# Kernel tuning notes

Measured on AMD Instinct MI355X. Metric: run time of the kernel, lower is better.

## Reference

```python
import jax, jax.numpy as jnp
import numpy as np

THETA = 128.0


def _make_Q(d, units):
    # Q[n,m] = (2n+1)/sqrt(d) if n > m and (n+m) odd, else 0 (fixed, non-trainable)
    n = np.arange(d)[:, None]
    m = np.arange(units)[None, :]
    Q = np.where((n > m) & (((n + m) % 2) == 1), (2 * n + 1) / np.sqrt(d), 0.0)
    return jnp.asarray(Q, dtype=jnp.float32)


def setup_inputs() -> dict:
    key = jax.random.key(0)
    k1, k2, k3, k4 = jax.random.split(key, 4)
    B_, T, Din, d, units = 16, 4096, 128, 256, 256
    x = jax.random.normal(k1, (B_, T, Din), dtype=jnp.float32)
    A = jax.random.normal(k2, (d, d), dtype=jnp.float32) / np.sqrt(d)
    Bm = jax.random.normal(k3, (Din, d), dtype=jnp.float32) / np.sqrt(Din)
    W_mix = jax.random.normal(k4, (units, units), dtype=jnp.float32) / np.sqrt(units)
    b_mix = jnp.zeros((units,), dtype=jnp.float32)
    return {"x": x, "A": A, "B": Bm, "W_mix": W_mix, "b_mix": b_mix}


def reference(x, A, B, W_mix, b_mix):
    d = A.shape[0]
    units = W_mix.shape[0]
    Q = _make_Q(d, units)
    QW = Q @ W_mix  # fuse fixed projection with dense kernel: (d, units)
    alpha = 1.0 - 1.0 / THETA
    beta = 1.0 / THETA
    # precompute input projection for all steps: (T, batch, d)
    xB = jnp.einsum('bti,id->tbd', x, B)

    def step(state, xBt):
        new_state = alpha * state + beta * (state @ A + xBt)
        y = jnp.tanh(new_state @ QW + b_mix)
        return new_state, y

    s0 = jnp.zeros((x.shape[0], d), dtype=x.dtype)
    _, ys = jax.lax.scan(step, s0, xB)  # ys: (T, batch, units)
    return jnp.transpose(ys, (1, 0, 2))
```

## Files before the change

### kernel.cpp

```cpp
#include <hip/hip_runtime.h>
#include <math.h>

constexpr int T_   = 4096;
constexpr int NB   = 16;
constexpr int D_   = 256;
constexpr int DIN  = 128;
constexpr int U_   = 256;
constexpr int L1   = 8;
constexpr int C1   = T_ / L1;
constexpr float ALPHA_ = 1.0f - 1.0f / 128.0f;
constexpr float BETA_  = 1.0f / 128.0f;
constexpr int SD   = NB * D_;
constexpr int MS   = D_ * D_;
constexpr int TLP  = D_ + 4;
constexpr int XLP  = DIN + 4;

using short8  = __attribute__((ext_vector_type(8))) short;
using float4v = __attribute__((ext_vector_type(4))) float;

__device__ __forceinline__ unsigned short bf16_rne(float x) {
  const unsigned b = __float_as_uint(x);
  const unsigned r = ((b >> 16) & 1u) + 0x7FFFu;
  return (unsigned short)((b + r) >> 16);
}
__device__ __forceinline__ float bf16_f(unsigned short h) {
  return __uint_as_float(((unsigned)h) << 16);
}

__device__ __forceinline__ void split2(float e0, float e1, unsigned& hd, unsigned& ld) {
  const unsigned b0 = __float_as_uint(e0), b1 = __float_as_uint(e1);
  const unsigned h0 = b0 & 0xFFFF0000u, h1 = b1 & 0xFFFF0000u;
  const float l0 = e0 - __uint_as_float(h0);
  const float l1 = e1 - __uint_as_float(h1);
  hd = (h0 >> 16) | h1;
  ld = (__float_as_uint(l0) >> 16) | (__float_as_uint(l1) & 0xFFFF0000u);
}

__device__ __forceinline__ void unpack8(uint4 a, uint4 b, short8& hi, short8& lo) {
  union { short8 s; unsigned u[4]; } H, L;
  const unsigned d[8] = {a.x, a.y, a.z, a.w, b.x, b.y, b.z, b.w};
#pragma unroll
  for (int i = 0; i < 4; ++i) {
    H.u[i] = (d[2 * i] >> 16) | (d[2 * i + 1] & 0xFFFF0000u);
    L.u[i] = (d[2 * i] & 0xFFFFu) | (d[2 * i + 1] << 16);
  }
  hi = H.s; lo = L.s;
}

__device__ __forceinline__ void mm_row(const float* __restrict__ Am,
                                       const float* __restrict__ Bm,
                                       float* __restrict__ Dm,
                                       int i, int tid, float* srow) {
  srow[tid] = Am[i * D_ + tid];
  __syncthreads();
  float a0 = 0.f, a1 = 0.f, a2 = 0.f, a3 = 0.f;
#pragma unroll 8
  for (int k = 0; k < D_; k += 4) {
    a0 = fmaf(srow[k + 0], Bm[(k + 0) * D_ + tid], a0);
    a1 = fmaf(srow[k + 1], Bm[(k + 1) * D_ + tid], a1);
    a2 = fmaf(srow[k + 2], Bm[(k + 2) * D_ + tid], a2);
    a3 = fmaf(srow[k + 3], Bm[(k + 3) * D_ + tid], a3);
  }
  Dm[i * D_ + tid] = (a0 + a1) + (a2 + a3);
  __syncthreads();
}

__global__ __launch_bounds__(256) void k_prep(const float* __restrict__ A,
                                              const float* __restrict__ W,
                                              float* __restrict__ Meff,
                                              float* __restrict__ QW,
                                              const float* __restrict__ Bm,
                                              unsigned short* __restrict__ Mf,
                                              unsigned short* __restrict__ Bmf) {
  const int bid = blockIdx.x, tid = threadIdx.x;
  if (bid < D_) {
    float v = BETA_ * A[bid * D_ + tid];
    if (bid == tid) v += ALPHA_;
    Meff[bid * D_ + tid] = v;
    return;
  }
  if (bid == D_) {
    __shared__ float wch[32 * D_];
    float se = 0.f, so = 0.f;
    for (int ch = 0; ch < D_ / 32; ++ch) {
      __syncthreads();
      for (int idx = tid; idx < 32 * D_; idx += 256)
        wch[idx] = W[ch * 32 * D_ + idx];
      __syncthreads();
#pragma unroll
      for (int r = 0; r < 32; ++r) {
        const int n = ch * 32 + r;
        const float sum = (n & 1) ? se : so;
        QW[n * U_ + tid] = sum * ((float)(2 * n + 1) / 16.0f);
        const float wv = wch[r * D_ + tid];
        if (n & 1) so += wv; else se += wv;
      }
    }
    return;
  }
  const int pb = bid - D_ - 1;
  const int lane = tid & 63, nb0 = tid >> 6;
  const int quad = lane >> 4, m16 = lane & 15;
  if (pb < 8) {
    const int ks = pb;
    for (int nb = nb0; nb < 16; nb += 4) {
      const size_t fo = ((size_t)(nb * 8 + ks) * 64 + lane) * 8;
#pragma unroll
      for (int jj = 0; jj < 8; ++jj) {
        const int k = ks * 32 + quad * 8 + jj;
        const int n = nb * 16 + m16;
        const float v = BETA_ * A[k * D_ + n];
        const unsigned short h = bf16_rne(v);
        Mf[fo + jj] = h;
        Mf[MS + fo + jj] = bf16_rne(v - bf16_f(h));
      }
    }
  } else {
    const int ks = pb - 8;
    unsigned short* dh = Bmf;
    unsigned short* dl = Bmf + (MS / 2);
    for (int nb = nb0; nb < 16; nb += 4) {
      const size_t fo = ((size_t)(nb * 4 + ks) * 64 + lane) * 8;
#pragma unroll
      for (int jj = 0; jj < 8; ++jj) {
        const int k = ks * 32 + quad * 8 + jj;
        const int n = nb * 16 + m16;
        const float v = BETA_ * Bm[k * D_ + n];
        const unsigned short h = bf16_rne(v);
        dh[fo + jj] = h;
        dl[fo + jj] = bf16_rne(v - bf16_f(h));
      }
    }
  }
}

__global__ __launch_bounds__(256) void k_pw(const float* __restrict__ Am,
                                            const float* __restrict__ Bbase,
                                            float* __restrict__ Dbase) {
  __shared__ float srow[D_];
  const int q = blockIdx.x >> 8, row = blockIdx.x & 255;
  mm_row(Am, Bbase + (size_t)q * MS, Dbase + (size_t)q * MS, row, threadIdx.x, srow);
}

__global__ __launch_bounds__(256) void k_pwr(const float* __restrict__ Abase,
                                             const float* __restrict__ Bm,
                                             float* __restrict__ Dbase) {
  __shared__ float srow[D_];
  const int q = blockIdx.x >> 8, row = blockIdx.x & 255;
  mm_row(Abase + (size_t)q * MS, Bm, Dbase + (size_t)q * MS, row, threadIdx.x, srow);
}

__global__ __launch_bounds__(512, 4) void k_big2(
    const float* __restrict__ R, const float* __restrict__ QWm,
    const float* __restrict__ M8, unsigned short* __restrict__ Bf,
    unsigned short* __restrict__ Pf0,
    const float* __restrict__ x, const unsigned short* __restrict__ Bmf,
    const unsigned short* __restrict__ Mf,
    unsigned short* __restrict__ Shi, unsigned short* __restrict__ Slo,
    float* __restrict__ Ends) {
  const int bid = blockIdx.x, tid = threadIdx.x;
  if (bid < 80) {
    const int mat = bid >> 3, ks = bid & 7;
    const float* X = (mat < 8) ? (R + (size_t)mat * MS) : (mat == 8 ? QWm : M8);
    unsigned short* dh = (mat < 9) ? (Bf + (size_t)mat * (2 * MS)) : Pf0;
    unsigned short* dl = dh + MS;
    const int lane = tid & 63, nb0 = tid >> 6;
    const int quad = lane >> 4, m16 = lane & 15;
    for (int nb = nb0; nb < 16; nb += 8) {
      const size_t fo = ((size_t)(nb * 8 + ks) * 64 + lane) * 8;
#pragma unroll
      for (int jj = 0; jj < 8; ++jj) {
        const int k = ks * 32 + quad * 8 + jj;
        const int n = nb * 16 + m16;
        const float xv = X[k * D_ + n];
        const unsigned short h = bf16_rne(xv);
        dh[fo + jj] = h;
        dl[fo + jj] = bf16_rne(xv - bf16_f(h));
      }
    }
    return;
  }
  __shared__ __align__(16) float xls[NB][XLP];
  __shared__ __align__(16) unsigned tls[NB][TLP];
  const int c = bid - 80;
  const int w = tid >> 6, lane = tid & 63;
  const int m16 = lane & 15, q = lane >> 4;
  const int xrow = tid >> 5, xi0 = (tid & 31) * 4;

  float4v sC[2];
#pragma unroll
  for (int nt = 0; nt < 2; ++nt) sC[nt] = (float4v){0.f, 0.f, 0.f, 0.f};

  for (int j = 0; j < L1; ++j) {
    const int t = c * L1 + j;
    __syncthreads();
    {
      const float* xr = x + ((size_t)xrow * T_ + t) * DIN + xi0;
      *(float4*)(&xls[xrow][xi0]) = *(const float4*)(xr);
    }
    if (j > 0) {
#pragma unroll
      for (int nt = 0; nt < 2; ++nt) {
        const int n = (w * 2 + nt) * 16 + m16;
#pragma unroll
        for (int r = 0; r < 4; ++r) {
          const float sv = sC[nt][r];
          const unsigned hb = __float_as_uint(sv) & 0xFFFF0000u;
          const float lo = sv - __uint_as_float(hb);
          tls[4 * q + r][n] = hb | (__float_as_uint(lo) >> 16);
        }
      }
    }
    __syncthreads();
    float4v acc[2];
#pragma unroll
    for (int nt = 0; nt < 2; ++nt) {
      acc[nt][0] = ALPHA_ * sC[nt][0];
      acc[nt][1] = ALPHA_ * sC[nt][1];
      acc[nt][2] = ALPHA_ * sC[nt][2];
      acc[nt][3] = ALPHA_ * sC[nt][3];
    }
#pragma unroll
    for (int ks = 0; ks < 4; ++ks) {
      float xv[8];
      *(float4*)(xv)     = *(const float4*)(&xls[m16][32 * ks + 8 * q]);
      *(float4*)(xv + 4) = *(const float4*)(&xls[m16][32 * ks + 8 * q + 4]);
      union { short8 s; unsigned u[4]; } XH, XL;
#pragma unroll
      for (int p = 0; p < 4; ++p) split2(xv[2 * p], xv[2 * p + 1], XH.u[p], XL.u[p]);
#pragma unroll
      for (int nt = 0; nt < 2; ++nt) {
        const size_t fo = ((size_t)((w * 2 + nt) * 4 + ks) * 64 + lane) * 8;
        const short8 bh = *(const short8*)(Bmf + fo);
        const short8 bl = *(const short8*)(Bmf + (MS / 2) + fo);
        acc[nt] = __builtin_amdgcn_mfma_f32_16x16x32_bf16(XH.s, bh, acc[nt], 0, 0, 0);
        acc[nt] = __builtin_amdgcn_mfma_f32_16x16x32_bf16(XH.s, bl, acc[nt], 0, 0, 0);
        acc[nt] = __builtin_amdgcn_mfma_f32_16x16x32_bf16(XL.s, bh, acc[nt], 0, 0, 0);
      }
    }
    if (j > 0) {
#pragma unroll
      for (int ks = 0; ks < 8; ++ks) {
        const uint4 p0 = *(const uint4*)(&tls[m16][32 * ks + 8 * q]);
        const uint4 p1 = *(const uint4*)(&tls[m16][32 * ks + 8 * q + 4]);
        short8 sh, sl; unpack8(p0, p1, sh, sl);
        if (ks == w) {
          const size_t ao = ((size_t)((t - 1) * 8 + ks) * 64 + lane) * 8;
          *(short8*)(Shi + ao) = sh;
          *(short8*)(Slo + ao) = sl;
        }
#pragma unroll
        for (int nt = 0; nt < 2; ++nt) {
          const size_t fo = ((size_t)((w * 2 + nt) * 8 + ks) * 64 + lane) * 8;
          const short8 mh = *(const short8*)(Mf + fo);
          const short8 ml = *(const short8*)(Mf + MS + fo);
          acc[nt] = __builtin_amdgcn_mfma_f32_16x16x32_bf16(sh, mh, acc[nt], 0, 0, 0);
          acc[nt] = __builtin_amdgcn_mfma_f32_16x16x32_bf16(sh, ml, acc[nt], 0, 0, 0);
          acc[nt] = __builtin_amdgcn_mfma_f32_16x16x32_bf16(sl, mh, acc[nt], 0, 0, 0);
        }
      }
    }
#pragma unroll
    for (int nt = 0; nt < 2; ++nt) sC[nt] = acc[nt];
  }
  const int tl = c * L1 + L1 - 1;
  __syncthreads();
#pragma unroll
  for (int nt = 0; nt < 2; ++nt) {
    const int n = (w * 2 + nt) * 16 + m16;
#pragma unroll
    for (int r = 0; r < 4; ++r) {
      const float sv = sC[nt][r];
      const unsigned hb = __float_as_uint(sv) & 0xFFFF0000u;
      const float lo = sv - __uint_as_float(hb);
      tls[4 * q + r][n] = hb | (__float_as_uint(lo) >> 16);
    }
  }
  __syncthreads();
  {
    const int ks = w;
    const uint4 p0 = *(const uint4*)(&tls[m16][32 * ks + 8 * q]);
    const uint4 p1 = *(const uint4*)(&tls[m16][32 * ks + 8 * q + 4]);
    short8 sh, sl; unpack8(p0, p1, sh, sl);
    const size_t ao = ((size_t)(tl * 8 + ks) * 64 + lane) * 8;
    *(short8*)(Shi + ao) = sh;
    *(short8*)(Slo + ao) = sl;
  }
#pragma unroll
  for (int nt = 0; nt < 2; ++nt) {
    const int n = (w * 2 + nt) * 16 + m16;
#pragma unroll
    for (int r = 0; r < 4; ++r)
      Ends[(size_t)c * SD + (size_t)(4 * q + r) * D_ + n] = sC[nt][r];
  }
}

__global__ __launch_bounds__(256) void k_scan(
    const float* __restrict__ Vin, float* __restrict__ Vout,
    const unsigned short* __restrict__ Pf,
    const float* __restrict__ Pf32,
    float* __restrict__ Psq,
    unsigned short* __restrict__ PfNext,
    int shift, int do_sq, int packmode,
    unsigned short* __restrict__ Hhi, unsigned short* __restrict__ Hlo) {
  __shared__ __align__(16) float smem[16 * TLP];
  const int bid = blockIdx.x, tid = threadIdx.x;
  if (bid >= C1) {
    if (!do_sq) return;
    const int i = bid - C1;
    smem[tid] = Pf32[i * D_ + tid];
    __syncthreads();
    float a0 = 0.f, a1 = 0.f, a2 = 0.f, a3 = 0.f;
#pragma unroll 8
    for (int k = 0; k < D_; k += 4) {
      a0 = fmaf(smem[k + 0], Pf32[(k + 0) * D_ + tid], a0);
      a1 = fmaf(smem[k + 1], Pf32[(k + 1) * D_ + tid], a1);
      a2 = fmaf(smem[k + 2], Pf32[(k + 2) * D_ + tid], a2);
      a3 = fmaf(smem[k + 3], Pf32[(k + 3) * D_ + tid], a3);
    }
    const float v = (a0 + a1) + (a2 + a3);
    Psq[i * D_ + tid] = v;
    const unsigned short h = bf16_rne(v);
    const unsigned short l = bf16_rne(v - bf16_f(h));
    const size_t off = ((size_t)((tid >> 4) * 8 + (i >> 5)) * 64 +
                        ((i >> 3) & 3) * 16 + (tid & 15)) * 8 + (i & 7);
    PfNext[off] = h;
    PfNext[MS + off] = l;
    return;
  }
  const int c = bid;
  const int w = tid >> 6, lane = tid & 63;
  const int m16 = lane & 15, q = lane >> 4;
  float4v acc[4];
#pragma unroll
  for (int nt = 0; nt < 4; ++nt) {
    const int n = (w * 4 + nt) * 16 + m16;
#pragma unroll
    for (int r = 0; r < 4; ++r)
      acc[nt][r] = Vin[(size_t)c * SD + (size_t)(4 * q + r) * D_ + n];
  }
  if (c >= shift) {
    const float* src = Vin + (size_t)(c - shift) * SD;
    {
      const int row = tid >> 4, col0 = (tid & 15) * 16;
#pragma unroll
      for (int p = 0; p < 4; ++p)
        *(float4*)(&smem[row * TLP + col0 + 4 * p]) =
            *(const float4*)(src + (size_t)row * D_ + col0 + 4 * p);
    }
    __syncthreads();
#pragma unroll
    for (int ks = 0; ks < 8; ++ks) {
      float xv[8];
      *(float4*)(xv)     = *(const float4*)(&smem[m16 * TLP + 32 * ks + 8 * q]);
      *(float4*)(xv + 4) = *(const float4*)(&smem[m16 * TLP + 32 * ks + 8 * q + 4]);
      union { short8 s; unsigned u[4]; } XH, XL;
#pragma unroll
      for (int p = 0; p < 4; ++p) split2(xv[2 * p], xv[2 * p + 1], XH.u[p], XL.u[p]);
#pragma unroll
      for (int nt = 0; nt < 4; ++nt) {
        const size_t fo = ((size_t)((w * 4 + nt) * 8 + ks) * 64 + lane) * 8;
        const short8 ph = *(const short8*)(Pf + fo);
        const short8 pl = *(const short8*)(Pf + MS + fo);
        acc[nt] = __builtin_amdgcn_mfma_f32_16x16x32_bf16(XH.s, ph, acc[nt], 0, 0, 0);
        acc[nt] = __builtin_amdgcn_mfma_f32_16x16x32_bf16(XH.s, pl, acc[nt], 0, 0, 0);
        acc[nt] = __builtin_amdgcn_mfma_f32_16x16x32_bf16(XL.s, ph, acc[nt], 0, 0, 0);
      }
    }
  }
  if (packmode) {
    __syncthreads();
    unsigned* tls = (unsigned*)smem;
#pragma unroll
    for (int nt = 0; nt < 4; ++nt) {
      const int n = (w * 4 + nt) * 16 + m16;
#pragma unroll
      for (int r = 0; r < 4; ++r) {
        const float sv = acc[nt][r];
        const unsigned hb = __float_as_uint(sv) & 0xFFFF0000u;
        const float lo = sv - __uint_as_float(hb);
        tls[(4 * q + r) * TLP + n] = hb | (__float_as_uint(lo) >> 16);
      }
    }
    __syncthreads();
#pragma unroll
    for (int ks = 0; ks < 8; ++ks) {
      const uint4 p0 = *(const uint4*)(&tls[m16 * TLP + 32 * ks + 8 * q]);
      const uint4 p1 = *(const uint4*)(&tls[m16 * TLP + 32 * ks + 8 * q + 4]);
      short8 sh, sl; unpack8(p0, p1, sh, sl);
      const size_t ao = ((size_t)(c * 8 + ks) * 64 + lane) * 8;
      *(short8*)(Hhi + ao) = sh;
      *(short8*)(Hlo + ao) = sl;
    }
  } else {
#pragma unroll
    for (int nt = 0; nt < 4; ++nt) {
      const int n = (w * 4 + nt) * 16 + m16;
#pragma unroll
      for (int r = 0; r < 4; ++r)
        Vout[(size_t)c * SD + (size_t)(4 * q + r) * D_ + n] = acc[nt][r];
    }
  }
}

__global__ __launch_bounds__(256, 3) void k_passB(
    const unsigned short* __restrict__ Shi, const unsigned short* __restrict__ Slo,
    const unsigned short* __restrict__ Hhi, const unsigned short* __restrict__ Hlo,
    const unsigned short* __restrict__ Bf, const float* __restrict__ bmix,
    float* __restrict__ out) {
  const int bid = blockIdx.x;
  const int g4 = (bid >> 3) * 4, j = bid & 7;
  const int tid = threadIdx.x;
  const int w = tid >> 6, lane = tid & 63;
  const int m16 = lane & 15, quad = lane >> 4;
  const unsigned short* Qh = Bf + (size_t)8 * 2 * MS;
  const unsigned short* Ql = Qh + MS;
  const unsigned short* Rh = Bf + (size_t)j * 2 * MS;
  const unsigned short* Rl = Rh + MS;

  float4v acc[4][4];
#pragma unroll
  for (int ci = 0; ci < 4; ++ci)
#pragma unroll
    for (int nt = 0; nt < 4; ++nt) acc[ci][nt] = (float4v){0.f, 0.f, 0.f, 0.f};

  for (int ks = 0; ks < 8; ++ks) {
    short8 fh[4], fl[4];
#pragma unroll
    for (int nt = 0; nt < 4; ++nt) {
      const size_t fo = ((size_t)((w * 4 + nt) * 8 + ks) * 64 + lane) * 8;
      fh[nt] = *(const short8*)(Qh + fo);
      fl[nt] = *(const short8*)(Ql + fo);
    }
#pragma unroll
    for (int ci = 0; ci < 4; ++ci) {
      const int t = (g4 + ci) * 8 + j;
      const size_t ao = ((size_t)(t * 8 + ks) * 64 + lane) * 8;
      const short8 sh = *(const short8*)(Shi + ao);
      const short8 sl = *(const short8*)(Slo + ao);
#pragma unroll
      for (int nt = 0; nt < 4; ++nt) {
        float4v a = acc[ci][nt];
        a = __builtin_amdgcn_mfma_f32_16x16x32_bf16(sh, fh[nt], a, 0, 0, 0);
        a = __builtin_amdgcn_mfma_f32_16x16x32_bf16(sh, fl[nt], a, 0, 0, 0);
        a = __builtin_amdgcn_mfma_f32_16x16x32_bf16(sl, fh[nt], a, 0, 0, 0);
        acc[ci][nt] = a;
      }
    }
#pragma unroll
    for (int nt = 0; nt < 4; ++nt) {
      const size_t fo = ((size_t)((w * 4 + nt) * 8 + ks) * 64 + lane) * 8;
      fh[nt] = *(const short8*)(Rh + fo);
      fl[nt] = *(const short8*)(Rl + fo);
    }
#pragma unroll
    for (int ci = 0; ci < 4; ++ci) {
      const int c = g4 + ci;
      if (c > 0) {
        const size_t ho = ((size_t)((c - 1) * 8 + ks) * 64 + lane) * 8;
        const short8 hh = *(const short8*)(Hhi + ho);
        const short8 hl = *(const short8*)(Hlo + ho);
#pragma unroll
        for (int nt = 0; nt < 4; ++nt) {
          float4v a = acc[ci][nt];
          a = __builtin_amdgcn_mfma_f32_16x16x32_bf16(hh, fh[nt], a, 0, 0, 0);
          a = __builtin_amdgcn_mfma_f32_16x16x32_bf16(hh, fl[nt], a, 0, 0, 0);
          a = __builtin_amdgcn_mfma_f32_16x16x32_bf16(hl, fh[nt], a, 0, 0, 0);
          acc[ci][nt] = a;
        }
      }
    }
  }
  __shared__ float ysm[16][U_ + 4];
  for (int ci = 0; ci < 4; ++ci) {
    const int t = (g4 + ci) * 8 + j;
    __syncthreads();
#pragma unroll
    for (int nt = 0; nt < 4; ++nt) {
      const int n = (w * 4 + nt) * 16 + m16;
      const float bias = bmix[n];
#pragma unroll
      for (int r = 0; r < 4; ++r) {
        const float v = acc[ci][nt][r] + bias;
        const float e = __expf(2.0f * v);
        ysm[quad * 4 + r][n] = 1.0f - 2.0f / (e + 1.0f);
      }
    }
    __syncthreads();
    for (int idx = tid; idx < 16 * (U_ / 4); idx += 256) {
      const int b = idx >> 6, c4 = (idx & 63) * 4;
      const float4 v = make_float4(ysm[b][c4], ysm[b][c4 + 1],
                                   ysm[b][c4 + 2], ysm[b][c4 + 3]);
      *(float4*)(out + ((size_t)b * T_ + t) * U_ + c4) = v;
    }
  }
}

extern "C" void kernel_launch(void* const* d_in, const int* in_sizes, int n_in,
                              void* d_out, int out_size, void* d_ws, size_t ws_size,
                              hipStream_t stream) {
  const float* x    = (const float*)d_in[0];
  const float* A    = (const float*)d_in[1];
  const float* Bm   = (const float*)d_in[2];
  const float* W    = (const float*)d_in[3];
  const float* bmix = (const float*)d_in[4];
  float* out = (float*)d_out;

  float* ws = (float*)d_ws;
  unsigned short* Shi = (unsigned short*)ws;
  unsigned short* Slo = (unsigned short*)(ws + 8388608);
  float* pw  = ws + 16777216;
  float* QW  = pw + 8 * (size_t)MS;
  float* R   = QW + MS;
  float* Sa  = R + 8 * (size_t)MS;
  float* Sb  = Sa + MS;
  unsigned short* Bf  = (unsigned short*)(Sb + MS);
  unsigned short* Mf  = Bf + (size_t)9 * 2 * MS;
  unsigned short* Bmf = Mf + 2 * (size_t)MS;
  unsigned short* Pf0 = Bmf + MS;
  unsigned short* Pf1 = Pf0 + 2 * (size_t)MS;
  (void)in_sizes; (void)n_in; (void)out_size; (void)ws_size;

  float* Va = out;
  float* Vb = out + (size_t)C1 * SD;

  unsigned short* Hhi = (unsigned short*)d_in[0];
  unsigned short* Hlo = Hhi + (size_t)C1 * 16 * 256;

  k_prep<<<D_ + 13, 256, 0, stream>>>(A, W, pw, QW, Bm, Mf, Bmf);
  k_pw<<<256, 256, 0, stream>>>(pw, pw, pw + MS);
  k_pw<<<512, 256, 0, stream>>>(pw + MS, pw, pw + 2 * (size_t)MS);
  k_pw<<<1024, 256, 0, stream>>>(pw + 3 * (size_t)MS, pw, pw + 4 * (size_t)MS);
  k_pwr<<<2048, 256, 0, stream>>>(pw, QW, R);
  k_big2<<<80 + C1, 512, 0, stream>>>(R, QW, pw + 7 * (size_t)MS, Bf, Pf0,
                                      x, Bmf, Mf, Shi, Slo, Va);

  const float* vin = Va; float* vout = Vb;
  const float* Pcur = pw + 7 * (size_t)MS;
  float* sqs[2] = {Sa, Sb};
  unsigned short* Pfp[2] = {Pf0, Pf1};
  for (int lvl = 0; lvl < 9; ++lvl) {
    float* Pd = sqs[lvl & 1];
    k_scan<<<C1 + D_, 256, 0, stream>>>(vin, vout, Pfp[lvl & 1], Pcur, Pd,
                                        Pfp[(lvl + 1) & 1], 1 << lvl,
                                        (lvl < 8) ? 1 : 0, (lvl == 8) ? 1 : 0,
                                        Hhi, Hlo);
    Pcur = Pd;
    const float* tmp = vin; vin = vout; vout = (float*)tmp;
  }

  k_passB<<<1024, 256, 0, stream>>>(Shi, Slo, Hhi, Hlo, Bf, bmix, out);
}
```

Baseline: 507.5 us.

## Process two chunks per block in chunk-local recurrence and skip finalized scan chunks

```diff
diff --git a/kernel.cpp b/kernel.cpp
--- a/kernel.cpp
+++ b/kernel.cpp
@@ -47,6 +47,13 @@
   hi = H.s; lo = L.s;
 }
 
+__device__ __forceinline__ int nwpar(int c, int l) {
+  if (c <= 0) return 0;
+  const int f = 31 - __clz(c);
+  const int nw = (l < f + 1) ? l : (f + 1);
+  return nw & 1;
+}
+
 __device__ __forceinline__ void mm_row(const float* __restrict__ Am,
                                        const float* __restrict__ Bm,
                                        float* __restrict__ Dm,
@@ -150,7 +157,7 @@
   mm_row(Abase + (size_t)q * MS, Bm, Dbase + (size_t)q * MS, row, threadIdx.x, srow);
 }
 
-__global__ __launch_bounds__(512, 4) void k_big2(
+__global__ __launch_bounds__(256, 2) void k_big2(
     const float* __restrict__ R, const float* __restrict__ QWm,
     const float* __restrict__ M8, unsigned short* __restrict__ Bf,
     unsigned short* __restrict__ Pf0,
@@ -166,7 +173,7 @@
     unsigned short* dl = dh + MS;
     const int lane = tid & 63, nb0 = tid >> 6;
     const int quad = lane >> 4, m16 = lane & 15;
-    for (int nb = nb0; nb < 16; nb += 8) {
+    for (int nb = nb0; nb < 16; nb += 4) {
       const size_t fo = ((size_t)(nb * 8 + ks) * 64 + lane) * 8;
 #pragma unroll
       for (int jj = 0; jj < 8; ++jj) {
@@ -180,134 +187,168 @@
     }
     return;
   }
-  __shared__ __align__(16) float xls[NB][XLP];
-  __shared__ __align__(16) unsigned tls[NB][TLP];
-  const int c = bid - 80;
+  __shared__ __align__(16) float xls[2][NB][XLP];
+  __shared__ __align__(16) unsigned tls[2][NB][TLP];
+  const int cc = bid - 80;
+  const int c0 = cc, c1 = cc + 256;
   const int w = tid >> 6, lane = tid & 63;
   const int m16 = lane & 15, q = lane >> 4;
-  const int xrow = tid >> 5, xi0 = (tid & 31) * 4;
-
-  float4v sC[2];
-#pragma unroll
-  for (int nt = 0; nt < 2; ++nt) sC[nt] = (float4v){0.f, 0.f, 0.f, 0.f};
+  const int xrow = tid >> 4, xi0 = (tid & 15) * 8;
+
+  float4v sC[2][4];
+#pragma unroll
+  for (int ch = 0; ch < 2; ++ch)
+#pragma unroll
+    for (int nt = 0; nt < 4; ++nt) sC[ch][nt] = (float4v){0.f, 0.f, 0.f, 0.f};
 
   for (int j = 0; j < L1; ++j) {
-    const int t = c * L1 + j;
     __syncthreads();
     {
-      const float* xr = x + ((size_t)xrow * T_ + t) * DIN + xi0;
-      *(float4*)(&xls[xrow][xi0]) = *(const float4*)(xr);
+      const float* xr0 = x + ((size_t)xrow * T_ + c0 * L1 + j) * DIN + xi0;
+      const float* xr1 = x + ((size_t)xrow * T_ + c1 * L1 + j) * DIN + xi0;
+      *(float4*)(&xls[0][xrow][xi0])     = *(const float4*)(xr0);
+      *(float4*)(&xls[0][xrow][xi0 + 4]) = *(const float4*)(xr0 + 4);
+      *(float4*)(&xls[1][xrow][xi0])     = *(const float4*)(xr1);
+      *(float4*)(&xls[1][xrow][xi0 + 4]) = *(const float4*)(xr1 + 4);
     }
     if (j > 0) {
 #pragma unroll
-      for (int nt = 0; nt < 2; ++nt) {
-        const int n = (w * 2 + nt) * 16 + m16;
-#pragma unroll
-        for (int r = 0; r < 4; ++r) {
-          const float sv = sC[nt][r];
-          const unsigned hb = __float_as_uint(sv) & 0xFFFF0000u;
-          const float lo = sv - __uint_as_float(hb);
-          tls[4 * q + r][n] = hb | (__float_as_uint(lo) >> 16);
+      for (int ch = 0; ch < 2; ++ch)
+#pragma unroll
+        for (int nt = 0; nt < 4; ++nt) {
+          const int n = (w * 4 + nt) * 16 + m16;
+#pragma unroll
+          for (int r = 0; r < 4; ++r) {
+            const float sv = sC[ch][nt][r];
+            const unsigned hb = __float_as_uint(sv) & 0xFFFF0000u;
+            const float lo = sv - __uint_as_float(hb);
+            tls[ch][4 * q + r][n] = hb | (__float_as_uint(lo) >> 16);
+          }
         }
-      }
-    }
-    __syncthreads();
-    float4v acc[2];
-#pragma unroll
-    for (int nt = 0; nt < 2; ++nt) {
-      acc[nt][0] = ALPHA_ * sC[nt][0];
-      acc[nt][1] = ALPHA_ * sC[nt][1];
-      acc[nt][2] = ALPHA_ * sC[nt][2];
-      acc[nt][3] = ALPHA_ * sC[nt][3];
-    }
+    }
+    __syncthreads();
+#pragma unroll
+    for (int ch = 0; ch < 2; ++ch)
+#pragma unroll
+      for (int nt = 0; nt < 4; ++nt) {
+        sC[ch][nt][0] *= ALPHA_; sC[ch][nt][1] *= ALPHA_;
+        sC[ch][nt][2] *= ALPHA_; sC[ch][nt][3] *= ALPHA_;
+      }
 #pragma unroll
     for (int ks = 0; ks < 4; ++ks) {
       float xv[8];
-      *(float4*)(xv)     = *(const float4*)(&xls[m16][32 * ks + 8 * q]);
-      *(float4*)(xv + 4) = *(const float4*)(&xls[m16][32 * ks + 8 * q + 4]);
-      union { short8 s; unsigned u[4]; } XH, XL;
-#pragma unroll
-      for (int p = 0; p < 4; ++p) split2(xv[2 * p], xv[2 * p + 1], XH.u[p], XL.u[p]);
-#pragma unroll
-      for (int nt = 0; nt < 2; ++nt) {
-        const size_t fo = ((size_t)((w * 2 + nt) * 4 + ks) * 64 + lane) * 8;
+      union { short8 s; unsigned u[4]; } XH0, XL0, XH1, XL1;
+      *(float4*)(xv)     = *(const float4*)(&xls[0][m16][32 * ks + 8 * q]);
+      *(float4*)(xv + 4) = *(const float4*)(&xls[0][m16][32 * ks + 8 * q + 4]);
+#pragma unroll
+      for (int p = 0; p < 4; ++p) split2(xv[2 * p], xv[2 * p + 1], XH0.u[p], XL0.u[p]);
+      *(float4*)(xv)     = *(const float4*)(&xls[1][m16][32 * ks + 8 * q]);
+      *(float4*)(xv + 4) = *(const float4*)(&xls[1][m16][32 * ks + 8 * q + 4]);
+#pragma unroll
+      for (int p = 0; p < 4; ++p) split2(xv[2 * p], xv[2 * p + 1], XH1.u[p], XL1.u[p]);
+#pragma unroll
+      for (int nt = 0; nt < 4; ++nt) {
+        const size_t fo = ((size_t)((w * 4 + nt) * 4 + ks) * 64 + lane) * 8;
         const short8 bh = *(const short8*)(Bmf + fo);
         const short8 bl = *(const short8*)(Bmf + (MS / 2) + fo);
-        acc[nt] = __builtin_amdgcn_mfma_f32_16x16x32_bf16(XH.s, bh, acc[nt], 0, 0, 0);
-        acc[nt] = __builtin_amdgcn_mfma_f32_16x16x32_bf16(XH.s, bl, acc[nt], 0, 0, 0);
-        acc[nt] = __builtin_amdgcn_mfma_f32_16x16x32_bf16(XL.s, bh, acc[nt], 0, 0, 0);
+        sC[0][nt] = __builtin_amdgcn_mfma_f32_16x16x32_bf16(XH0.s, bh, sC[0][nt], 0, 0, 0);
+        sC[0][nt] = __builtin_amdgcn_mfma_f32_16x16x32_bf16(XH0.s, bl, sC[0][nt], 0, 0, 0);
+        sC[0][nt] = __builtin_amdgcn_mfma_f32_16x16x32_bf16(XL0.s, bh, sC[0][nt], 0, 0, 0);
+        sC[1][nt] = __builtin_amdgcn_mfma_f32_16x16x32_bf16(XH1.s, bh, sC[1][nt], 0, 0, 0);
+        sC[1][nt] = __builtin_amdgcn_mfma_f32_16x16x32_bf16(XH1.s, bl, sC[1][nt], 0, 0, 0);
+        sC[1][nt] = __builtin_amdgcn_mfma_f32_16x16x32_bf16(XL1.s, bh, sC[1][nt], 0, 0, 0);
       }
     }
     if (j > 0) {
 #pragma unroll
       for (int ks = 0; ks < 8; ++ks) {
-        const uint4 p0 = *(const uint4*)(&tls[m16][32 * ks + 8 * q]);
-        const uint4 p1 = *(const uint4*)(&tls[m16][32 * ks + 8 * q + 4]);
-        short8 sh, sl; unpack8(p0, p1, sh, sl);
-        if (ks == w) {
-          const size_t ao = ((size_t)((t - 1) * 8 + ks) * 64 + lane) * 8;
-          *(short8*)(Shi + ao) = sh;
-          *(short8*)(Slo + ao) = sl;
+        const uint4 p00 = *(const uint4*)(&tls[0][m16][32 * ks + 8 * q]);
+        const uint4 p01 = *(const uint4*)(&tls[0][m16][32 * ks + 8 * q + 4]);
+        const uint4 p10 = *(const uint4*)(&tls[1][m16][32 * ks + 8 * q]);
+        const uint4 p11 = *(const uint4*)(&tls[1][m16][32 * ks + 8 * q + 4]);
+        short8 sh0, sl0, sh1, sl1;
+        unpack8(p00, p01, sh0, sl0);
+        unpack8(p10, p11, sh1, sl1);
+        if ((ks & 3) == w) {
+          const size_t a0 = ((size_t)((c0 * L1 + j - 1) * 8 + ks) * 64 + lane) * 8;
+          const size_t a1 = ((size_t)((c1 * L1 + j - 1) * 8 + ks) * 64 + lane) * 8;
+          *(short8*)(Shi + a0) = sh0;
+          *(short8*)(Slo + a0) = sl0;
+          *(short8*)(Shi + a1) = sh1;
+          *(short8*)(Slo + a1) = sl1;
         }
 #pragma unroll
-        for (int nt = 0; nt < 2; ++nt) {
-          const size_t fo = ((size_t)((w * 2 + nt) * 8 + ks) * 64 + lane) * 8;
+        for (int nt = 0; nt < 4; ++nt) {
+          const size_t fo = ((size_t)((w * 4 + nt) * 8 + ks) * 64 + lane) * 8;
           const short8 mh = *(const short8*)(Mf + fo);
           const short8 ml = *(const short8*)(Mf + MS + fo);
-          acc[nt] = __builtin_amdgcn_mfma_f32_16x16x32_bf16(sh, mh, acc[nt], 0, 0, 0);
-          acc[nt] = __builtin_amdgcn_mfma_f32_16x16x32_bf16(sh, ml, acc[nt], 0, 0, 0);
-          acc[nt] = __builtin_amdgcn_mfma_f32_16x16x32_bf16(sl, mh, acc[nt], 0, 0, 0);
+          sC[0][nt] = __builtin_amdgcn_mfma_f32_16x16x32_bf16(sh0, mh, sC[0][nt], 0, 0, 0);
+          sC[0][nt] = __builtin_amdgcn_mfma_f32_16x16x32_bf16(sh0, ml, sC[0][nt], 0, 0, 0);
+          sC[0][nt] = __builtin_amdgcn_mfma_f32_16x16x32_bf16(sl0, mh, sC[0][nt], 0, 0, 0);
+          sC[1][nt] = __builtin_amdgcn_mfma_f32_16x16x32_bf16(sh1, mh, sC[1][nt], 0, 0, 0);
+          sC[1][nt] = __builtin_amdgcn_mfma_f32_16x16x32_bf16(sh1, ml, sC[1][nt], 0, 0, 0);
+          sC[1][nt] = __builtin_amdgcn_mfma_f32_16x16x32_bf16(sl1, mh, sC[1][nt], 0, 0, 0);
         }
       }
     }
-#pragma unroll
-    for (int nt = 0; nt < 2; ++nt) sC[nt] = acc[nt];
-  }
-  const int tl = c * L1 + L1 - 1;
+  }
   __syncthreads();
 #pragma unroll
-  for (int nt = 0; nt < 2; ++nt) {
-    const int n = (w * 2 + nt) * 16 + m16;
-#pragma unroll
-    for (int r = 0; r < 4; ++r) {
-      const float sv = sC[nt][r];
-      const unsigned hb = __float_as_uint(sv) & 0xFFFF0000u;
-      const float lo = sv - __uint_as_float(hb);
-      tls[4 * q + r][n] = hb | (__float_as_uint(lo) >> 16);
-    }
-  }
+  for (int ch = 0; ch < 2; ++ch)
+#pragma unroll
+    for (int nt = 0; nt < 4; ++nt) {
+      const int n = (w * 4 + nt) * 16 + m16;
+#pragma unroll
+      for (int r = 0; r < 4; ++r) {
+        const float sv = sC[ch][nt][r];
+        const unsigned hb = __float_as_uint(sv) & 0xFFFF0000u;
+        const float lo = sv - __uint_as_float(hb);
+        tls[ch][4 * q + r][n] = hb | (__float_as_uint(lo) >> 16);
+      }
+    }
   __syncthreads();
-  {
-    const int ks = w;
-    const uint4 p0 = *(const uint4*)(&tls[m16][32 * ks + 8 * q]);
-    const uint4 p1 = *(const uint4*)(&tls[m16][32 * ks + 8 * q + 4]);
-    short8 sh, sl; unpack8(p0, p1, sh, sl);
-    const size_t ao = ((size_t)(tl * 8 + ks) * 64 + lane) * 8;
-    *(short8*)(Shi + ao) = sh;
-    *(short8*)(Slo + ao) = sl;
-  }
-#pragma unroll
-  for (int nt = 0; nt < 2; ++nt) {
-    const int n = (w * 2 + nt) * 16 + m16;
-#pragma unroll
-    for (int r = 0; r < 4; ++r)
-      Ends[(size_t)c * SD + (size_t)(4 * q + r) * D_ + n] = sC[nt][r];
+#pragma unroll
+  for (int kk = 0; kk < 2; ++kk) {
+    const int ks = w + kk * 4;
+#pragma unroll
+    for (int ch = 0; ch < 2; ++ch) {
+      const int tl = (ch == 0 ? c0 : c1) * L1 + L1 - 1;
+      const uint4 p0 = *(const uint4*)(&tls[ch][m16][32 * ks + 8 * q]);
+      const uint4 p1 = *(const uint4*)(&tls[ch][m16][32 * ks + 8 * q + 4]);
+      short8 sh, sl; unpack8(p0, p1, sh, sl);
+      const size_t ao = ((size_t)(tl * 8 + ks) * 64 + lane) * 8;
+      *(short8*)(Shi + ao) = sh;
+      *(short8*)(Slo + ao) = sl;
+    }
+  }
+#pragma unroll
+  for (int ch = 0; ch < 2; ++ch) {
+    const int c = (ch == 0) ? c0 : c1;
+#pragma unroll
+    for (int nt = 0; nt < 4; ++nt) {
+      const int n = (w * 4 + nt) * 16 + m16;
+#pragma unroll
+      for (int r = 0; r < 4; ++r)
+        Ends[(size_t)c * SD + (size_t)(4 * q + r) * D_ + n] = sC[ch][nt][r];
+    }
   }
 }
 
 __global__ __launch_bounds__(256) void k_scan(
-    const float* __restrict__ Vin, float* __restrict__ Vout,
+    float* V0, float* V1,
     const unsigned short* __restrict__ Pf,
     const float* __restrict__ Pf32,
     float* __restrict__ Psq,
     unsigned short* __restrict__ PfNext,
-    int shift, int do_sq, int packmode,
+    int lvl, int do_sq, int packmode,
     unsigned short* __restrict__ Hhi, unsigned short* __restrict__ Hlo) {
   __shared__ __align__(16) float smem[16 * TLP];
   const int bid = blockIdx.x, tid = threadIdx.x;
-  if (bid >= C1) {
+  const int shift = 1 << lvl;
+  const int Cw = packmode ? C1 : (C1 - shift);
+  if (bid >= Cw) {
     if (!do_sq) return;
-    const int i = bid - C1;
+    const int i = bid - Cw;
     smem[tid] = Pf32[i * D_ + tid];
     __syncthreads();
     float a0 = 0.f, a1 = 0.f, a2 = 0.f, a3 = 0.f;
@@ -328,19 +369,22 @@
     PfNext[MS + off] = l;
     return;
   }
-  const int c = bid;
+  const int c = packmode ? bid : (bid + shift);
   const int w = tid >> 6, lane = tid & 63;
   const int m16 = lane & 15, q = lane >> 4;
+  const int ownPar = nwpar(c, lvl);
+  const float* Vown = ownPar ? V1 : V0;
   float4v acc[4];
 #pragma unroll
   for (int nt = 0; nt < 4; ++nt) {
     const int n = (w * 4 + nt) * 16 + m16;
 #pragma unroll
     for (int r = 0; r < 4; ++r)
-      acc[nt][r] = Vin[(size_t)c * SD + (size_t)(4 * q + r) * D_ + n];
+      acc[nt][r] = Vown[(size_t)c * SD + (size_t)(4 * q + r) * D_ + n];
   }
   if (c >= shift) {
-    const float* src = Vin + (size_t)(c - shift) * SD;
+    const float* Vsrc = nwpar(c - shift, lvl) ? V1 : V0;
+    const float* src = Vsrc + (size_t)(c - shift) * SD;
     {
       const int row = tid >> 4, col0 = (tid & 15) * 16;
 #pragma unroll
@@ -393,12 +437,13 @@
       *(short8*)(Hlo + ao) = sl;
     }
   } else {
+    float* Vdst = (ownPar ^ 1) ? V1 : V0;
 #pragma unroll
     for (int nt = 0; nt < 4; ++nt) {
       const int n = (w * 4 + nt) * 16 + m16;
 #pragma unroll
       for (int r = 0; r < 4; ++r)
-        Vout[(size_t)c * SD + (size_t)(4 * q + r) * D_ + n] = acc[nt][r];
+        Vdst[(size_t)c * SD + (size_t)(4 * q + r) * D_ + n] = acc[nt][r];
     }
   }
 }
@@ -521,8 +566,8 @@
   unsigned short* Pf1 = Pf0 + 2 * (size_t)MS;
   (void)in_sizes; (void)n_in; (void)out_size; (void)ws_size;
 
-  float* Va = out;
-  float* Vb = out + (size_t)C1 * SD;
+  float* V0 = out;
+  float* V1 = out + (size_t)C1 * SD;
 
   unsigned short* Hhi = (unsigned short*)d_in[0];
   unsigned short* Hlo = Hhi + (size_t)C1 * 16 * 256;
@@ -532,21 +577,21 @@
   k_pw<<<512, 256, 0, stream>>>(pw + MS, pw, pw + 2 * (size_t)MS);
   k_pw<<<1024, 256, 0, stream>>>(pw + 3 * (size_t)MS, pw, pw + 4 * (size_t)MS);
   k_pwr<<<2048, 256, 0, stream>>>(pw, QW, R);
-  k_big2<<<80 + C1, 512, 0, stream>>>(R, QW, pw + 7 * (size_t)MS, Bf, Pf0,
-                                      x, Bmf, Mf, Shi, Slo, Va);
-
-  const float* vin = Va; float* vout = Vb;
+  k_big2<<<80 + 256, 256, 0, stream>>>(R, QW, pw + 7 * (size_t)MS, Bf, Pf0,
+                                       x, Bmf, Mf, Shi, Slo, V0);
+
   const float* Pcur = pw + 7 * (size_t)MS;
   float* sqs[2] = {Sa, Sb};
   unsigned short* Pfp[2] = {Pf0, Pf1};
   for (int lvl = 0; lvl < 9; ++lvl) {
     float* Pd = sqs[lvl & 1];
-    k_scan<<<C1 + D_, 256, 0, stream>>>(vin, vout, Pfp[lvl & 1], Pcur, Pd,
-                                        Pfp[(lvl + 1) & 1], 1 << lvl,
-                                        (lvl < 8) ? 1 : 0, (lvl == 8) ? 1 : 0,
-                                        Hhi, Hlo);
+    const int pack = (lvl == 8) ? 1 : 0;
+    const int do_sq = (lvl < 8) ? 1 : 0;
+    const int grid = pack ? C1 : (C1 - (1 << lvl)) + D_;
+    k_scan<<<grid, 256, 0, stream>>>(V0, V1, Pfp[lvl & 1], Pcur, Pd,
+                                     Pfp[(lvl + 1) & 1], lvl, do_sq, pack,
+                                     Hhi, Hlo);
     Pcur = Pd;
-    const float* tmp = vin; vin = vout; vout = (float*)tmp;
   }
 
   k_passB<<<1024, 256, 0, stream>>>(Shi, Slo, Hhi, Hlo, Bf, bmix, out);
```

After: 467.3 us. 1.09x faster.
